# Kernel tuning notes

Measured on AMD Instinct MI355X. Metric: run time of the kernel, lower is better.

## Reference

```python
import jax, jax.numpy as jnp
import numpy as np

N = 131072
K = 27
FIN = 3
FOUT = 32
EPS = 1e-5


def _bn(h, gamma, beta, mean, var):
    return (h - mean) * jax.lax.rsqrt(var + EPS) * gamma + beta


def setup_inputs() -> dict:
    key = jax.random.key(0)
    ks = jax.random.split(key, 8)
    return {
        "x_feats": jax.random.normal(ks[0], (N, FIN), jnp.float32),
        "z_feats": jax.random.normal(ks[1], (N, FIN), jnp.float32),
        "nbr_idx": jax.random.randint(ks[2], (N, K), 0, N, jnp.int32),
        "w1": jax.random.normal(ks[3], (K, FIN, FOUT), jnp.float32) * 0.2,
        "bn1_gamma": jnp.ones((FOUT,), jnp.float32),
        "bn1_beta": jnp.zeros((FOUT,), jnp.float32),
        "bn1_mean": jax.random.normal(ks[4], (FOUT,), jnp.float32) * 0.1,
        "bn1_var": jax.random.uniform(ks[5], (FOUT,), jnp.float32, 0.5, 1.5),
        "w2": jax.random.normal(ks[6], (K, FOUT, FOUT), jnp.float32) * 0.1,
        "mlp_w": jax.random.normal(ks[7], (FIN, FOUT), jnp.float32) * 0.3,
        "mlp_b": jnp.zeros((FOUT,), jnp.float32),
        "mlp_gamma": jnp.ones((FOUT,), jnp.float32),
        "mlp_beta": jnp.zeros((FOUT,), jnp.float32),
        "mlp_mean": jnp.zeros((FOUT,), jnp.float32),
        "mlp_var": jnp.ones((FOUT,), jnp.float32),
    }


def reference(x_feats, z_feats, nbr_idx, w1, bn1_gamma, bn1_beta, bn1_mean,
              bn1_var, w2, mlp_w, mlp_b, mlp_gamma, mlp_beta, mlp_mean,
              mlp_var):
    # --- voxel branch: sparse conv (gather-GEMM) -> BN -> SiLU -> sparse conv
    g1 = x_feats[nbr_idx]                       # [N, K, FIN] irregular gather
    h = jnp.einsum('nkf,kfo->no', g1, w1)       # [N, FOUT]
    h = jax.nn.silu(_bn(h, bn1_gamma, bn1_beta, bn1_mean, bn1_var))
    g2 = h[nbr_idx]                             # [N, K, FOUT] irregular gather
    x_out = jnp.einsum('nkf,kfo->no', g2, w2)   # [N, FOUT]

    # --- point branch: SharedMLP = Linear -> BN -> ReLU
    z = z_feats @ mlp_w + mlp_b
    z = jax.nn.relu(_bn(z, mlp_gamma, mlp_beta, mlp_mean, mlp_var))

    # --- mixed_mix: fuse voxel and point features additively
    fused = x_out + z
    return (fused, fused)
```

## Files before the change

kernel.cpp:

```cpp
#include <hip/hip_runtime.h>
#include <math.h>

#define NN 131072
#define KK 27
#define FIN 3
#define FOUT 32
#define EPS 1e-5f

typedef _Float16 f16;
typedef __attribute__((ext_vector_type(8))) _Float16 f16x8;
typedef __attribute__((ext_vector_type(4)))  float   f32x4;
typedef __attribute__((ext_vector_type(16))) float   f32x16;

__device__ __forceinline__ void pack_w2_block(
    const float* __restrict__ w2, f16* __restrict__ w2p, int k, int t)
{
#pragma unroll
    for (int r = 0; r < 4; ++r) {
        const int e    = r * 256 + t;
        const int half = e >> 9;
        const int l    = (e >> 3) & 63;
        const int j    = e & 7;
        const int krow = half * 16 + ((l >> 5) << 3) + j;
        const int n    = l & 31;
        w2p[k * 1024 + e] = (f16)w2[k * (FOUT * FOUT) + krow * FOUT + n];
    }
}

__global__ __launch_bounds__(256) void conv1_pack_kernel(
    const float* __restrict__ x_feats,
    const int*   __restrict__ nbr_idx,
    const float* __restrict__ w1,
    const float* __restrict__ g1,  const float* __restrict__ b1,
    const float* __restrict__ m1,  const float* __restrict__ v1,
    f16* __restrict__ h_out,
    const float* __restrict__ w2, f16* __restrict__ w2p)
{
    if (blockIdx.x >= NN / 256) {
        pack_w2_block(w2, w2p, blockIdx.x - NN / 256, threadIdx.x);
        return;
    }
    const int n = blockIdx.x * 256 + threadIdx.x;

    int idxs[KK];
    const int* nb = nbr_idx + (size_t)n * KK;
#pragma unroll
    for (int k = 0; k < KK; ++k) idxs[k] = nb[k];

    float acc[FOUT];
#pragma unroll
    for (int o = 0; o < FOUT; ++o) acc[o] = 0.f;

#pragma unroll
    for (int c = 0; c < 3; ++c) {
        float xs[9][3];
#pragma unroll
        for (int q = 0; q < 9; ++q) {
            const float* xr = x_feats + (size_t)idxs[c * 9 + q] * FIN;
            xs[q][0] = xr[0]; xs[q][1] = xr[1]; xs[q][2] = xr[2];
        }
#pragma unroll
        for (int q = 0; q < 9; ++q) {
            const float* w = w1 + (c * 9 + q) * (FIN * FOUT);
#pragma unroll
            for (int o = 0; o < FOUT; ++o) {
                float a = acc[o];
                a = fmaf(xs[q][0], w[o],            a);
                a = fmaf(xs[q][1], w[FOUT + o],     a);
                a = fmaf(xs[q][2], w[2 * FOUT + o], a);
                acc[o] = a;
            }
        }
    }

    f16* hr = h_out + (size_t)n * FOUT;
#pragma unroll
    for (int g = 0; g < 4; ++g) {
        f16x8 hv;
#pragma unroll
        for (int j = 0; j < 8; ++j) {
            const int o = g * 8 + j;
            const float sc = g1[o] * rsqrtf(v1[o] + EPS);
            float v = (acc[o] - m1[o]) * sc + b1[o];
            v = v / (1.f + __expf(-v));
            hv[j] = (f16)v;
        }
        *(f16x8*)(hr + g * 8) = hv;
    }
}

__global__ __launch_bounds__(256) void conv2_mfma_kernel(
    const f16*   __restrict__ h,
    const int*   __restrict__ nbr_idx,
    const f16*   __restrict__ w2p,
    const float* __restrict__ z_feats,
    const float* __restrict__ mlp_w,
    const float* __restrict__ mlp_b,
    const float* __restrict__ mg, const float* __restrict__ mbe,
    const float* __restrict__ mm, const float* __restrict__ mv,
    float* __restrict__ out)
{
    const int lane = threadIdx.x & 63;
    const int wave = threadIdx.x >> 6;
    const int base = (blockIdx.x * 4 + wave) * 32;
    const int row  = lane & 31;
    const int hi   = lane >> 5;

    int idxs[KK];
    const int* nb = nbr_idx + (size_t)(base + row) * KK;
#pragma unroll
    for (int k = 0; k < KK; ++k) idxs[k] = nb[k];
#pragma unroll
    for (int k = 0; k < KK; ++k) asm volatile("" : "+v"(idxs[k]));

    f32x16 acc0 = {};
    f32x16 acc1 = {};

    f32x4 wa1[6], wa2[6], wb1[6], wb2[6];

#define C2_ISSUE(t, s) do {                                                  \
        const f16* hr_ = h + (size_t)idxs[t] * FOUT + hi * 8;                \
        const f16* bb_ = w2p + (t) * 1024 + lane * 8;                        \
        asm volatile("global_load_dwordx4 %0, %1, off"                       \
                     : "=v"(wa1[s]) : "v"(hr_));                             \
        asm volatile("global_load_dwordx4 %0, %1, off"                       \
                     : "=v"(wa2[s]) : "v"(hr_ + 16));                        \
        asm volatile("global_load_dwordx4 %0, %1, off"                       \
                     : "=v"(wb1[s]) : "v"(bb_));                             \
        asm volatile("global_load_dwordx4 %0, %1, off"                       \
                     : "=v"(wb2[s]) : "v"(bb_ + 512));                       \
    } while (0)

#pragma unroll
    for (int t = 0; t < 6; ++t) C2_ISSUE(t, t);

#pragma unroll
    for (int k = 0; k < KK; ++k) {
        const int rem = KK - 1 - k;
        if      (rem >= 5) asm volatile("s_waitcnt vmcnt(20)");
        else if (rem == 4) asm volatile("s_waitcnt vmcnt(16)");
        else if (rem == 3) asm volatile("s_waitcnt vmcnt(12)");
        else if (rem == 2) asm volatile("s_waitcnt vmcnt(8)");
        else if (rem == 1) asm volatile("s_waitcnt vmcnt(4)");
        else               asm volatile("s_waitcnt vmcnt(0)");
        __builtin_amdgcn_sched_barrier(0);

        const int s = k % 6;
        const f16x8 a1 = __builtin_bit_cast(f16x8, wa1[s]);
        const f16x8 a2 = __builtin_bit_cast(f16x8, wa2[s]);
        const f16x8 b1 = __builtin_bit_cast(f16x8, wb1[s]);
        const f16x8 b2 = __builtin_bit_cast(f16x8, wb2[s]);
        __builtin_amdgcn_s_setprio(1);
        acc0 = __builtin_amdgcn_mfma_f32_32x32x16_f16(a1, b1, acc0, 0, 0, 0);
        acc1 = __builtin_amdgcn_mfma_f32_32x32x16_f16(a2, b2, acc1, 0, 0, 0);
        __builtin_amdgcn_s_setprio(0);

        if (k + 6 < KK) C2_ISSUE(k + 6, s);
    }
#undef C2_ISSUE

    const int n0 = lane & 31;
    const float wc0 = mlp_w[n0];
    const float wc1 = mlp_w[FOUT + n0];
    const float wc2 = mlp_w[2 * FOUT + n0];
    const float sc  = mg[n0] * rsqrtf(mv[n0] + EPS);
    const float bi  = mlp_b[n0];
    const float mmv = mm[n0];
    const float mbv = mbe[n0];

#pragma unroll
    for (int r = 0; r < 16; ++r) {
        const int m    = (r & 3) + ((r >> 2) << 3) + (hi << 2);
        const int node = base + m;
        const float* zr = z_feats + (size_t)node * FIN;
        float z = bi;
        z = fmaf(zr[0], wc0, z);
        z = fmaf(zr[1], wc1, z);
        z = fmaf(zr[2], wc2, z);
        z = (z - mmv) * sc + mbv;
        z = fmaxf(z, 0.f);
        const float v = acc0[r] + acc1[r] + z;
        out[(size_t)node * FOUT + n0] = v;
        out[(size_t)NN * FOUT + (size_t)node * FOUT + n0] = v;
    }
}

extern "C" void kernel_launch(void* const* d_in, const int* in_sizes, int n_in,
                              void* d_out, int out_size, void* d_ws, size_t ws_size,
                              hipStream_t stream) {
    const float* x_feats = (const float*)d_in[0];
    const float* z_feats = (const float*)d_in[1];
    const int*   nbr_idx = (const int*)d_in[2];
    const float* w1      = (const float*)d_in[3];
    const float* bn1_g   = (const float*)d_in[4];
    const float* bn1_b   = (const float*)d_in[5];
    const float* bn1_m   = (const float*)d_in[6];
    const float* bn1_v   = (const float*)d_in[7];
    const float* w2      = (const float*)d_in[8];
    const float* mlp_w   = (const float*)d_in[9];
    const float* mlp_b   = (const float*)d_in[10];
    const float* mlp_g   = (const float*)d_in[11];
    const float* mlp_be  = (const float*)d_in[12];
    const float* mlp_m   = (const float*)d_in[13];
    const float* mlp_v   = (const float*)d_in[14];

    f16* h   = (f16*)d_ws;
    f16* w2p = (f16*)((char*)d_ws + (size_t)8 * 1024 * 1024);
    float* out = (float*)d_out;

    conv1_pack_kernel<<<NN / 256 + KK, 256, 0, stream>>>(
        x_feats, nbr_idx, w1, bn1_g, bn1_b, bn1_m, bn1_v, h, w2, w2p);
    conv2_mfma_kernel<<<NN / 128, 256, 0, stream>>>(
        h, nbr_idx, w2p, z_feats, mlp_w, mlp_b, mlp_g, mlp_be,
        mlp_m, mlp_v, out);
}
```

Measured before the change: 169.1 us.

## Software-pipeline conv1 neighbor gathers with inline asm loads and waitcnts

```diff
diff --git a/kernel.cpp b/kernel.cpp
--- a/kernel.cpp
+++ b/kernel.cpp
@@ -27,7 +27,7 @@
     }
 }
 
-__global__ __launch_bounds__(256) void conv1_pack_kernel(
+__global__ __launch_bounds__(256, 2) void conv1_pack_kernel(
     const float* __restrict__ x_feats,
     const int*   __restrict__ nbr_idx,
     const float* __restrict__ w1,
@@ -46,32 +46,61 @@
     const int* nb = nbr_idx + (size_t)n * KK;
 #pragma unroll
     for (int k = 0; k < KK; ++k) idxs[k] = nb[k];
+#pragma unroll
+    for (int k = 0; k < KK; ++k) asm volatile("" : "+v"(idxs[k]));
 
     float acc[FOUT];
 #pragma unroll
     for (int o = 0; o < FOUT; ++o) acc[o] = 0.f;
 
-#pragma unroll
-    for (int c = 0; c < 3; ++c) {
-        float xs[9][3];
-#pragma unroll
-        for (int q = 0; q < 9; ++q) {
-            const float* xr = x_feats + (size_t)idxs[c * 9 + q] * FIN;
-            xs[q][0] = xr[0]; xs[q][1] = xr[1]; xs[q][2] = xr[2];
+    float xw[14][3];
+
+#define C1_ISSUE(tap, s) do {                                                \
+        const float* p_ = x_feats + (size_t)idxs[tap] * FIN;                 \
+        asm volatile("global_load_dword %0, %1, off"                         \
+                     : "=v"(xw[s][0]) : "v"(p_));                            \
+        asm volatile("global_load_dword %0, %1, off offset:4"                \
+                     : "=v"(xw[s][1]) : "v"(p_));                            \
+        asm volatile("global_load_dword %0, %1, off offset:8"                \
+                     : "=v"(xw[s][2]) : "v"(p_));                            \
+    } while (0)
+
+#pragma unroll
+    for (int t = 0; t < 7; ++t) C1_ISSUE(t, t);
+
+#pragma unroll
+    for (int c = 0; c < 4; ++c) {
+        const int cs  = (c < 3) ? 7 : 6;
+        if (c + 1 < 4) {
+            const int ns = (c + 1 < 3) ? 7 : 6;
+#pragma unroll
+            for (int q = 0; q < 7; ++q)
+                if (q < ns) C1_ISSUE((c + 1) * 7 + q, ((c + 1) * 7 + q) % 14);
         }
-#pragma unroll
-        for (int q = 0; q < 9; ++q) {
-            const float* w = w1 + (c * 9 + q) * (FIN * FOUT);
-#pragma unroll
-            for (int o = 0; o < FOUT; ++o) {
-                float a = acc[o];
-                a = fmaf(xs[q][0], w[o],            a);
-                a = fmaf(xs[q][1], w[FOUT + o],     a);
-                a = fmaf(xs[q][2], w[2 * FOUT + o], a);
-                acc[o] = a;
+        if      (c == 0) asm volatile("s_waitcnt vmcnt(21)");
+        else if (c == 1) asm volatile("s_waitcnt vmcnt(21)");
+        else if (c == 2) asm volatile("s_waitcnt vmcnt(18)");
+        else             asm volatile("s_waitcnt vmcnt(0)");
+        __builtin_amdgcn_sched_barrier(0);
+
+#pragma unroll
+        for (int q = 0; q < 7; ++q) {
+            if (q < cs) {
+                const int tap = c * 7 + q;
+                const int s   = tap % 14;
+                const float* w = w1 + tap * (FIN * FOUT);
+#pragma unroll
+                for (int o = 0; o < FOUT; ++o) {
+                    float a = acc[o];
+                    a = fmaf(xw[s][0], w[o],            a);
+                    a = fmaf(xw[s][1], w[FOUT + o],     a);
+                    a = fmaf(xw[s][2], w[2 * FOUT + o], a);
+                    acc[o] = a;
+                }
             }
         }
     }
+#undef C1_ISSUE
 
     f16* hr = h_out + (size_t)n * FOUT;
 #pragma unroll
@@ -89,7 +118,7 @@
     }
 }
 
-__global__ __launch_bounds__(256) void conv2_mfma_kernel(
+__global__ __launch_bounds__(256, 2) void conv2_mfma_kernel(
     const f16*   __restrict__ h,
     const int*   __restrict__ nbr_idx,
     const f16*   __restrict__ w2p,
@@ -123,12 +152,12 @@
         const f16* bb_ = w2p + (t) * 1024 + lane * 8;                        \
         asm volatile("global_load_dwordx4 %0, %1, off"                       \
                      : "=v"(wa1[s]) : "v"(hr_));                             \
-        asm volatile("global_load_dwordx4 %0, %1, off"                       \
-                     : "=v"(wa2[s]) : "v"(hr_ + 16));                        \
+        asm volatile("global_load_dwordx4 %0, %1, off offset:32"             \
+                     : "=v"(wa2[s]) : "v"(hr_));                             \
         asm volatile("global_load_dwordx4 %0, %1, off"                       \
                      : "=v"(wb1[s]) : "v"(bb_));                             \
-        asm volatile("global_load_dwordx4 %0, %1, off"                       \
-                     : "=v"(wb2[s]) : "v"(bb_ + 512));                       \
+        asm volatile("global_load_dwordx4 %0, %1, off offset:1024"           \
+                     : "=v"(wb2[s]) : "v"(bb_));                             \
     } while (0)
 
 #pragma unroll
```

New measurement: 169.2 us. Within noise of the previous version (+0.1%).

## Pad x to float4, pipeline conv1 gathers, stage w2 in LDS

Applied to the files above, without the earlier changes.

```diff
diff --git a/kernel.cpp b/kernel.cpp
--- a/kernel.cpp
+++ b/kernel.cpp
@@ -12,66 +12,90 @@
 typedef __attribute__((ext_vector_type(4)))  float   f32x4;
 typedef __attribute__((ext_vector_type(16))) float   f32x16;
 
-__device__ __forceinline__ void pack_w2_block(
-    const float* __restrict__ w2, f16* __restrict__ w2p, int k, int t)
-{
-#pragma unroll
-    for (int r = 0; r < 4; ++r) {
-        const int e    = r * 256 + t;
-        const int half = e >> 9;
-        const int l    = (e >> 3) & 63;
-        const int j    = e & 7;
-        const int krow = half * 16 + ((l >> 5) << 3) + j;
-        const int n    = l & 31;
-        w2p[k * 1024 + e] = (f16)w2[k * (FOUT * FOUT) + krow * FOUT + n];
-    }
-}
-
-__global__ __launch_bounds__(256) void conv1_pack_kernel(
-    const float* __restrict__ x_feats,
-    const int*   __restrict__ nbr_idx,
-    const float* __restrict__ w1,
-    const float* __restrict__ g1,  const float* __restrict__ b1,
-    const float* __restrict__ m1,  const float* __restrict__ v1,
-    f16* __restrict__ h_out,
+__global__ __launch_bounds__(256) void prep_kernel(
+    const float* __restrict__ x, float4* __restrict__ xp,
     const float* __restrict__ w2, f16* __restrict__ w2p)
 {
     if (blockIdx.x >= NN / 256) {
-        pack_w2_block(w2, w2p, blockIdx.x - NN / 256, threadIdx.x);
+        const int k = blockIdx.x - NN / 256;
+        const int t = threadIdx.x;
+#pragma unroll
+        for (int r = 0; r < 4; ++r) {
+            const int e    = r * 256 + t;
+            const int half = e >> 9;
+            const int l    = (e >> 3) & 63;
+            const int j    = e & 7;
+            const int krow = half * 16 + ((l >> 5) << 3) + j;
+            const int n    = l & 31;
+            w2p[k * 1024 + e] = (f16)w2[k * (FOUT * FOUT) + krow * FOUT + n];
+        }
         return;
     }
+    const int n = blockIdx.x * 256 + threadIdx.x;
+    const float* r = x + (size_t)n * 3;
+    xp[n] = make_float4(r[0], r[1], r[2], 0.f);
+}
+
+__global__ __launch_bounds__(256, 2) void conv1_kernel(
+    const float4* __restrict__ xpad,
+    const int*    __restrict__ nbr_idx,
+    const float*  __restrict__ w1,
+    const float* __restrict__ g1,  const float* __restrict__ b1,
+    const float* __restrict__ m1,  const float* __restrict__ v1,
+    f16* __restrict__ h_out)
+{
     const int n = blockIdx.x * 256 + threadIdx.x;
 
     int idxs[KK];
     const int* nb = nbr_idx + (size_t)n * KK;
 #pragma unroll
     for (int k = 0; k < KK; ++k) idxs[k] = nb[k];
+#pragma unroll
+    for (int k = 0; k < KK; ++k) asm volatile("" : "+v"(idxs[k]));
 
     float acc[FOUT];
 #pragma unroll
     for (int o = 0; o < FOUT; ++o) acc[o] = 0.f;
 
-#pragma unroll
-    for (int c = 0; c < 3; ++c) {
-        float xs[9][3];
-#pragma unroll
-        for (int q = 0; q < 9; ++q) {
-            const float* xr = x_feats + (size_t)idxs[c * 9 + q] * FIN;
-            xs[q][0] = xr[0]; xs[q][1] = xr[1]; xs[q][2] = xr[2];
-        }
-#pragma unroll
-        for (int q = 0; q < 9; ++q) {
-            const float* w = w1 + (c * 9 + q) * (FIN * FOUT);
-#pragma unroll
-            for (int o = 0; o < FOUT; ++o) {
-                float a = acc[o];
-                a = fmaf(xs[q][0], w[o],            a);
-                a = fmaf(xs[q][1], w[FOUT + o],     a);
-                a = fmaf(xs[q][2], w[2 * FOUT + o], a);
-                acc[o] = a;
-            }
-        }
-    }
+    f32x4 xw[9];
+
+#define C1_ISSUE(tap, s) do {                                                \
+        const float4* p_ = xpad + idxs[tap];                                 \
+        asm volatile("global_load_dwordx4 %0, %1, off"                       \
+                     : "=v"(xw[s]) : "v"(p_));                               \
+    } while (0)
+
+#pragma unroll
+    for (int t = 0; t < 9; ++t) C1_ISSUE(t, t);
+
+#pragma unroll
+    for (int k = 0; k < KK; ++k) {
+        const int rem = KK - 1 - k;
+        if      (rem >= 8) asm volatile("s_waitcnt vmcnt(8)");
+        else if (rem == 7) asm volatile("s_waitcnt vmcnt(7)");
+        else if (rem == 6) asm volatile("s_waitcnt vmcnt(6)");
+        else if (rem == 5) asm volatile("s_waitcnt vmcnt(5)");
+        else if (rem == 4) asm volatile("s_waitcnt vmcnt(4)");
+        else if (rem == 3) asm volatile("s_waitcnt vmcnt(3)");
+        else if (rem == 2) asm volatile("s_waitcnt vmcnt(2)");
+        else if (rem == 1) asm volatile("s_waitcnt vmcnt(1)");
+        else               asm volatile("s_waitcnt vmcnt(0)");
+        __builtin_amdgcn_sched_barrier(0);
+
+        const int s = k % 9;
+        const float xx = xw[s].x, xy = xw[s].y, xz = xw[s].z;
+        const float* w = w1 + k * (FIN * FOUT);
+#pragma unroll
+        for (int o = 0; o < FOUT; ++o) {
+            float a = acc[o];
+            a = fmaf(xx, w[o],            a);
+            a = fmaf(xy, w[FOUT + o],     a);
+            a = fmaf(xz, w[2 * FOUT + o], a);
+            acc[o] = a;
+        }
+        if (k + 9 < KK) C1_ISSUE(k + 9, s);
+    }
+#undef C1_ISSUE
 
     f16* hr = h_out + (size_t)n * FOUT;
 #pragma unroll
@@ -89,7 +113,7 @@
     }
 }
 
-__global__ __launch_bounds__(256) void conv2_mfma_kernel(
+__global__ __launch_bounds__(256, 2) void conv2_mfma_kernel(
     const f16*   __restrict__ h,
     const int*   __restrict__ nbr_idx,
     const f16*   __restrict__ w2p,
@@ -100,8 +124,20 @@
     const float* __restrict__ mm, const float* __restrict__ mv,
     float* __restrict__ out)
 {
-    const int lane = threadIdx.x & 63;
-    const int wave = threadIdx.x >> 6;
+    __shared__ f16 bsm[KK * 1024];
+
+    const int t = threadIdx.x;
+    {
+        const f32x4* src = (const f32x4*)w2p;
+        f32x4*       dst = (f32x4*)bsm;
+#pragma unroll
+        for (int i = 0; i < 13; ++i) dst[i * 256 + t] = src[i * 256 + t];
+        if (t < 128) dst[3328 + t] = src[3328 + t];
+    }
+    __syncthreads();
+
+    const int lane = t & 63;
+    const int wave = t >> 6;
     const int base = (blockIdx.x * 4 + wave) * 32;
     const int row  = lane & 31;
     const int hi   = lane >> 5;
@@ -116,46 +152,50 @@
     f32x16 acc0 = {};
     f32x16 acc1 = {};
 
-    f32x4 wa1[6], wa2[6], wb1[6], wb2[6];
-
-#define C2_ISSUE(t, s) do {                                                  \
-        const f16* hr_ = h + (size_t)idxs[t] * FOUT + hi * 8;                \
-        const f16* bb_ = w2p + (t) * 1024 + lane * 8;                        \
+    f32x4 wa1[6], wa2[6];
+
+#define C2_ISSUE(tp, s) do {                                                 \
+        const f16* hr_ = h + (size_t)idxs[tp] * FOUT + hi * 8;               \
         asm volatile("global_load_dwordx4 %0, %1, off"                       \
                      : "=v"(wa1[s]) : "v"(hr_));                             \
-        asm volatile("global_load_dwordx4 %0, %1, off"                       \
-                     : "=v"(wa2[s]) : "v"(hr_ + 16));                        \
-        asm volatile("global_load_dwordx4 %0, %1, off"                       \
-                     : "=v"(wb1[s]) : "v"(bb_));                             \
-        asm volatile("global_load_dwordx4 %0, %1, off"                       \
-                     : "=v"(wb2[s]) : "v"(bb_ + 512));                       \
+        asm volatile("global_load_dwordx4 %0, %1, off offset:32"             \
+                     : "=v"(wa2[s]) : "v"(hr_));                             \
     } while (0)
 
 #pragma unroll
-    for (int t = 0; t < 6; ++t) C2_ISSUE(t, t);
+    for (int p = 0; p < 6; ++p) C2_ISSUE(p, p);
+
+    const f16* bl = bsm + lane * 8;
+    f16x8 b1 = *(const f16x8*)bl;
+    f16x8 b2 = *(const f16x8*)(bl + 512);
 
 #pragma unroll
     for (int k = 0; k < KK; ++k) {
         const int rem = KK - 1 - k;
-        if      (rem >= 5) asm volatile("s_waitcnt vmcnt(20)");
-        else if (rem == 4) asm volatile("s_waitcnt vmcnt(16)");
-        else if (rem == 3) asm volatile("s_waitcnt vmcnt(12)");
-        else if (rem == 2) asm volatile("s_waitcnt vmcnt(8)");
-        else if (rem == 1) asm volatile("s_waitcnt vmcnt(4)");
+        if      (rem >= 5) asm volatile("s_waitcnt vmcnt(10)");
+        else if (rem == 4) asm volatile("s_waitcnt vmcnt(8)");
+        else if (rem == 3) asm volatile("s_waitcnt vmcnt(6)");
+        else if (rem == 2) asm volatile("s_waitcnt vmcnt(4)");
+        else if (rem == 1) asm volatile("s_waitcnt vmcnt(2)");
         else               asm volatile("s_waitcnt vmcnt(0)");
         __builtin_amdgcn_sched_barrier(0);
+
+        f16x8 nb1, nb2;
+        if (k + 1 < KK) {
+            nb1 = *(const f16x8*)(bl + (k + 1) * 1024);
+            nb2 = *(const f16x8*)(bl + (k + 1) * 1024 + 512);
+        }
 
         const int s = k % 6;
         const f16x8 a1 = __builtin_bit_cast(f16x8, wa1[s]);
         const f16x8 a2 = __builtin_bit_cast(f16x8, wa2[s]);
-        const f16x8 b1 = __builtin_bit_cast(f16x8, wb1[s]);
-        const f16x8 b2 = __builtin_bit_cast(f16x8, wb2[s]);
         __builtin_amdgcn_s_setprio(1);
         acc0 = __builtin_amdgcn_mfma_f32_32x32x16_f16(a1, b1, acc0, 0, 0, 0);
         acc1 = __builtin_amdgcn_mfma_f32_32x32x16_f16(a2, b2, acc1, 0, 0, 0);
         __builtin_amdgcn_s_setprio(0);
 
         if (k + 6 < KK) C2_ISSUE(k + 6, s);
+        if (k + 1 < KK) { b1 = nb1; b2 = nb2; }
     }
 #undef C2_ISSUE
 
@@ -204,12 +244,14 @@
     const float* mlp_m   = (const float*)d_in[13];
     const float* mlp_v   = (const float*)d_in[14];
 
-    f16* h   = (f16*)d_ws;
-    f16* w2p = (f16*)((char*)d_ws + (size_t)8 * 1024 * 1024);
-    float* out = (float*)d_out;
-
-    conv1_pack_kernel<<<NN / 256 + KK, 256, 0, stream>>>(
-        x_feats, nbr_idx, w1, bn1_g, bn1_b, bn1_m, bn1_v, h, w2, w2p);
+    f16*    h    = (f16*)d_ws;
+    f16*    w2p  = (f16*)((char*)d_ws + (size_t)8 * 1024 * 1024);
+    float4* xpad = (float4*)((char*)d_ws + (size_t)9 * 1024 * 1024);
+    float*  out  = (float*)d_out;
+
+    prep_kernel<<<NN / 256 + KK, 256, 0, stream>>>(x_feats, xpad, w2, w2p);
+    conv1_kernel<<<NN / 256, 256, 0, stream>>>(
+        xpad, nbr_idx, w1, bn1_g, bn1_b, bn1_m, bn1_v, h);
     conv2_mfma_kernel<<<NN / 128, 256, 0, stream>>>(
         h, nbr_idx, w2p, z_feats, mlp_w, mlp_b, mlp_g, mlp_be,
         mlp_m, mlp_v, out);
```

Measured after the change: 188.4 us. 1.11x slower.
